# Optimization experiments

Hardware: AMD Instinct MI355X
Metric: run time of the kernel (lower is better)

Reference implementation:

```python
import jax, jax.numpy as jnp
import numpy as np

BIT_SHIFT = 8
H, W = 480, 640
N = 100000
C_IN, C_HID, C_OUT = 96, 576, 96


def setup_inputs() -> dict:
    key = jax.random.key(0)
    ks = jax.random.split(key, 12)
    # --- sparse 2D coordinates (unique active sites on an H x W grid) ---
    rng = np.random.default_rng(0)
    lin = rng.choice(H * W, size=N, replace=False)
    ys, xs = lin // W, lin % W
    grid = -np.ones((H, W), dtype=np.int32)
    grid[ys, xs] = np.arange(N, dtype=np.int32)
    # neighbor index for each of the 9 kernel offsets; -1 where no active neighbor
    nbr = np.empty((9, N), dtype=np.int32)
    k = 0
    for dy in (-1, 0, 1):
        for dx in (-1, 0, 1):
            yn, xn = ys + dy, xs + dx
            valid = (yn >= 0) & (yn < H) & (xn >= 0) & (xn < W)
            idx = grid[np.clip(yn, 0, H - 1), np.clip(xn, 0, W - 1)]
            nbr[k] = np.where(valid, idx, -1)
            k += 1
    # --- int8-valued float features / weights (quantized integer inference) ---
    feats = jnp.round(jnp.clip(30.0 * jax.random.normal(ks[0], (N, C_IN)), -127, 127))
    w1 = jnp.round(jnp.clip(40.0 * jax.random.normal(ks[1], (C_IN, C_HID)), -127, 127))
    b1 = jnp.round(1000.0 * jax.random.normal(ks[2], (C_HID,)))
    w2 = jnp.round(jnp.clip(40.0 * jax.random.normal(ks[3], (9, C_HID)), -127, 127))
    b2 = jnp.round(1000.0 * jax.random.normal(ks[4], (C_HID,)))
    w3 = jnp.round(jnp.clip(40.0 * jax.random.normal(ks[5], (C_HID, C_OUT)), -127, 127))
    b3 = jnp.round(1000.0 * jax.random.normal(ks[6], (C_OUT,)))
    # per-output-channel requantization scaling factors (>= ~1 so round() is nonzero)
    s1 = 1.0 + 3.0 * jax.random.uniform(ks[7], (C_HID,))
    s2 = 1.0 + 3.0 * jax.random.uniform(ks[8], (C_HID,))
    s3 = 1.0 + 3.0 * jax.random.uniform(ks[9], (C_OUT,))
    s_main = 1.0 + 2.0 * jax.random.uniform(ks[10], ())
    s_res = 1.0 + 2.0 * jax.random.uniform(ks[11], ())
    return {"feats": feats, "neighbor_idx": jnp.asarray(nbr), "w1": w1, "b1": b1,
            "w2": w2, "b2": b2, "w3": w3, "b3": b3,
            "s1": s1, "s2": s2, "s3": s3, "s_main": s_main, "s_res": s_res}


def _requant(acc, s):
    # fused integer rescale: multiplier m = round(s) * 2^bit_shift, then /2^(2*bit_shift)
    B = 2.0 ** BIT_SHIFT
    return acc * (jnp.round(s) * B) / (B * B)


def _clamp(x):
    lim = 2.0 ** (BIT_SHIFT - 1)
    return jnp.clip(x, -lim, lim)


def _relu6(x):
    return jnp.clip(x, 0.0, 6.0)


def reference(feats, neighbor_idx, w1, b1, w2, b2, w3, b3, s1, s2, s3, s_main, s_res):
    B = 2.0 ** BIT_SHIFT
    # 1x1 expand conv (dense GEMM over active sites)
    x = _relu6(_clamp(_requant(feats @ w1 + b1, s1)))  # [N, C_HID]
    # depthwise 3x3 sparse conv: gather 9 neighbor taps, mask missing sites
    mask = (neighbor_idx >= 0).astype(x.dtype)               # [9, N]
    gathered = x[jnp.clip(neighbor_idx, 0, None)] * mask[:, :, None]  # [9, N, C_HID]
    dw = jnp.einsum('knc,kc->nc', gathered, w2) + b2
    x = _relu6(_clamp(_requant(dw, s2)))
    # 1x1 project conv
    x = _clamp(_requant(x @ w3 + b3, s3))                    # [N, C_OUT]
    # scaled residual add
    out = jnp.round(s_main) * B * x + jnp.round(s_res) * B * feats
    return out
```

## Files before the change

### kernel.cpp

```cpp
#include <hip/hip_runtime.h>
#include <hip/hip_bf16.h>
#include <hip/hip_fp16.h>

#define NS   100000
#define CIN  96
#define CHID 576
#define COUT 96
#define SPB  48
#define LDH  (CHID + 8)
#define CPT  8
#define NG   (CHID / CPT)
#define NSLOT (576 / NG)
#define SPS  (SPB / NSLOT)

typedef float    floatx4 __attribute__((ext_vector_type(4)));
typedef int      intx4   __attribute__((ext_vector_type(4)));
typedef short    short8  __attribute__((ext_vector_type(8)));
typedef _Float16 half8   __attribute__((ext_vector_type(8)));
typedef _Float16 half4   __attribute__((ext_vector_type(4)));

__global__ void prep_kernel(const float* __restrict__ w1, const float* __restrict__ w3,
                            const float* __restrict__ w2,
                            unsigned short* __restrict__ w1T, _Float16* __restrict__ w3T,
                            _Float16* __restrict__ w2h, _Float16* __restrict__ x1h) {
  int i = blockIdx.x * blockDim.x + threadIdx.x;
  if (i >= CHID * CIN) return;
  if (i < CHID) x1h[(size_t)NS * CHID + i] = (_Float16)0.0f;
  if (i < 9 * CHID) w2h[i] = (_Float16)w2[i];
  {
    int h = i / CIN, k = i % CIN;
    w1T[i] = (unsigned short)(__float_as_uint(w1[k * CHID + h]) >> 16);
  }
  {
    int o = i / CHID, k = i % CHID;
    w3T[i] = (_Float16)w3[k * COUT + o];
  }
}

__global__ __launch_bounds__(64) void expand_kernel(
    const float* __restrict__ feats, const float* __restrict__ b1,
    const float* __restrict__ s1, const unsigned short* __restrict__ w1T,
    _Float16* __restrict__ x1h) {
  const int lane = threadIdx.x;
  const int m = lane & 15, quad = lane >> 4;
  const int s0 = blockIdx.x * 64;

  short8 bfrag[4][3];
#pragma unroll
  for (int u = 0; u < 4; ++u) {
    const int site = min(s0 + u * 16 + m, NS - 1);
    const float* frow = feats + (size_t)site * CIN + quad * 8;
#pragma unroll
    for (int kc = 0; kc < 3; ++kc) {
      const float4 lo = *reinterpret_cast<const float4*>(frow + kc * 32);
      const float4 hi = *reinterpret_cast<const float4*>(frow + kc * 32 + 4);
      const float v[8] = {lo.x, lo.y, lo.z, lo.w, hi.x, hi.y, hi.z, hi.w};
#pragma unroll
      for (int j = 0; j < 8; ++j)
        bfrag[u][kc][j] = (short)(__float_as_uint(v[j]) >> 16);
    }
  }

  const int hq = quad * 4;
#pragma unroll 2
  for (int ht = 0; ht < CHID / 16; ++ht) {
    const unsigned short* wrow = w1T + (ht * 16 + m) * CIN + quad * 8;
    short8 a[3];
#pragma unroll
    for (int kc = 0; kc < 3; ++kc)
      a[kc] = *reinterpret_cast<const short8*>(wrow + kc * 32);

    floatx4 acc[4] = {{0.f, 0.f, 0.f, 0.f}, {0.f, 0.f, 0.f, 0.f},
                      {0.f, 0.f, 0.f, 0.f}, {0.f, 0.f, 0.f, 0.f}};
#pragma unroll
    for (int kc = 0; kc < 3; ++kc)
#pragma unroll
      for (int u = 0; u < 4; ++u)
        acc[u] = __builtin_amdgcn_mfma_f32_16x16x32_bf16(a[kc], bfrag[u][kc], acc[u], 0, 0, 0);

    const floatx4 bv = *reinterpret_cast<const floatx4*>(b1 + ht * 16 + hq);
    const floatx4 sv = *reinterpret_cast<const floatx4*>(s1 + ht * 16 + hq);
    floatx4 sc;
#pragma unroll
    for (int j = 0; j < 4; ++j) sc[j] = rintf(sv[j]) * (1.0f / 256.0f);

#pragma unroll
    for (int u = 0; u < 4; ++u) {
      const int site = s0 + u * 16 + m;
      if (site < NS) {
        half4 r;
#pragma unroll
        for (int j = 0; j < 4; ++j) {
          float v = (acc[u][j] + bv[j]) * sc[j];
          r[j] = (_Float16)fminf(fmaxf(v, 0.0f), 6.0f);
        }
        *reinterpret_cast<half4*>(x1h + (size_t)site * CHID + ht * 16 + hq) = r;
      }
    }
  }
}

__global__ __launch_bounds__(576) void dwproj_kernel(
    const int* __restrict__ nbr, const _Float16* __restrict__ w2h,
    const float* __restrict__ b2, const float* __restrict__ s2,
    const _Float16* __restrict__ x1h, const _Float16* __restrict__ w3T,
    const float* __restrict__ feats, const float* __restrict__ b3,
    const float* __restrict__ s3, const float* __restrict__ s_main,
    const float* __restrict__ s_res, float* __restrict__ out) {
  __shared__ _Float16 x2t[SPB * LDH];
  __shared__ int offt[SPB * 12];
  const int t = threadIdx.x;
  const int s0 = blockIdx.x * SPB;

  if (t < SPB * 9) {
    const int k = t / SPB, n = t - k * SPB;
    const int site = min(s0 + n, NS - 1);
    const int idx = nbr[k * NS + site];
    offt[n * 12 + k] = (idx < 0 ? NS : idx) * CHID;
  }
  __syncthreads();

  {
    const int g = t % NG;
    const int slot = t / NG;
    const int c0 = g * CPT;
    half8 wv[9];
#pragma unroll
    for (int k = 0; k < 9; ++k)
      wv[k] = *reinterpret_cast<const half8*>(w2h + k * CHID + c0);
    float bvv[8], scv[8];
    {
      const floatx4 b0 = *reinterpret_cast<const floatx4*>(b2 + c0);
      const floatx4 b1v = *reinterpret_cast<const floatx4*>(b2 + c0 + 4);
      const floatx4 sa = *reinterpret_cast<const floatx4*>(s2 + c0);
      const floatx4 sb = *reinterpret_cast<const floatx4*>(s2 + c0 + 4);
#pragma unroll
      for (int j = 0; j < 4; ++j) {
        bvv[j] = b0[j];     bvv[j + 4] = b1v[j];
        scv[j] = rintf(sa[j]) * (1.0f / 256.0f);
        scv[j + 4] = rintf(sb[j]) * (1.0f / 256.0f);
      }
    }
#pragma unroll 2
    for (int i = 0; i < SPS; ++i) {
      const int n = slot * SPS + i;
      const intx4 oa = *reinterpret_cast<const intx4*>(offt + n * 12);
      const intx4 ob = *reinterpret_cast<const intx4*>(offt + n * 12 + 4);
      const int o8 = offt[n * 12 + 8];
      half8 v0 = *reinterpret_cast<const half8*>(x1h + (size_t)oa.x + c0);
      half8 v1 = *reinterpret_cast<const half8*>(x1h + (size_t)oa.y + c0);
      half8 v2 = *reinterpret_cast<const half8*>(x1h + (size_t)oa.z + c0);
      half8 v3 = *reinterpret_cast<const half8*>(x1h + (size_t)oa.w + c0);
      half8 v4 = *reinterpret_cast<const half8*>(x1h + (size_t)ob.x + c0);
      half8 v5 = *reinterpret_cast<const half8*>(x1h + (size_t)ob.y + c0);
      half8 v6 = *reinterpret_cast<const half8*>(x1h + (size_t)ob.z + c0);
      half8 v7 = *reinterpret_cast<const half8*>(x1h + (size_t)ob.w + c0);
      half8 v8 = *reinterpret_cast<const half8*>(x1h + (size_t)o8 + c0);
      float acc[8];
#pragma unroll
      for (int j = 0; j < 8; ++j) acc[j] = bvv[j];
#pragma unroll
      for (int j = 0; j < 8; ++j) {
        acc[j] += (float)v0[j] * (float)wv[0][j];
        acc[j] += (float)v1[j] * (float)wv[1][j];
        acc[j] += (float)v2[j] * (float)wv[2][j];
        acc[j] += (float)v3[j] * (float)wv[3][j];
        acc[j] += (float)v4[j] * (float)wv[4][j];
        acc[j] += (float)v5[j] * (float)wv[5][j];
        acc[j] += (float)v6[j] * (float)wv[6][j];
        acc[j] += (float)v7[j] * (float)wv[7][j];
        acc[j] += (float)v8[j] * (float)wv[8][j];
      }
      half8 r;
#pragma unroll
      for (int j = 0; j < 8; ++j) {
        float v = acc[j] * scv[j];
        r[j] = (_Float16)fminf(fmaxf(v, 0.0f), 6.0f);
      }
      *reinterpret_cast<half8*>(x2t + n * LDH + c0) = r;
    }
  }
  __syncthreads();

  const int wave = t >> 6, lane = t & 63;
  const int m = lane & 15, quad = lane >> 4;
  const float rsm = rintf(s_main[0]) * 256.0f;
  const float rsr = rintf(s_res[0]) * 256.0f;

  for (int tile = wave; tile < (SPB / 16) * (COUT / 16); tile += 9) {
    const int tm = tile / (COUT / 16);
    const int ot = tile % (COUT / 16);
    floatx4 acc = {0.f, 0.f, 0.f, 0.f};
    const _Float16* arow = w3T + (ot * 16 + m) * CHID + quad * 8;
    const _Float16* blds = x2t + (tm * 16 + m) * LDH + quad * 8;
#pragma unroll
    for (int kc = 0; kc < 18; ++kc) {
      const half8 a = *reinterpret_cast<const half8*>(arow + kc * 32);
      const half8 b = *reinterpret_cast<const half8*>(blds + kc * 32);
      acc = __builtin_amdgcn_mfma_f32_16x16x32_f16(a, b, acc, 0, 0, 0);
    }
    const int site = s0 + tm * 16 + m;
    if (site < NS) {
      const int o0 = ot * 16 + quad * 4;
      const floatx4 b3v = *reinterpret_cast<const floatx4*>(b3 + o0);
      const floatx4 s3v = *reinterpret_cast<const floatx4*>(s3 + o0);
      const floatx4 fv =
          *reinterpret_cast<const floatx4*>(feats + (size_t)site * COUT + o0);
      floatx4 r;
#pragma unroll
      for (int j = 0; j < 4; ++j) {
        float v = (acc[j] + b3v[j]) * (rintf(s3v[j]) * (1.0f / 256.0f));
        v = fminf(fmaxf(v, -128.0f), 128.0f);
        r[j] = rsm * v + rsr * fv[j];
      }
      *reinterpret_cast<floatx4*>(out + (size_t)site * COUT + o0) = r;
    }
  }
}

extern "C" void kernel_launch(void* const* d_in, const int* in_sizes, int n_in,
                              void* d_out, int out_size, void* d_ws, size_t ws_size,
                              hipStream_t stream) {
  const float* feats  = (const float*)d_in[0];
  const int*   nbr    = (const int*)d_in[1];
  const float* w1     = (const float*)d_in[2];
  const float* b1     = (const float*)d_in[3];
  const float* w2     = (const float*)d_in[4];
  const float* b2     = (const float*)d_in[5];
  const float* w3     = (const float*)d_in[6];
  const float* b3     = (const float*)d_in[7];
  const float* s1     = (const float*)d_in[8];
  const float* s2     = (const float*)d_in[9];
  const float* s3     = (const float*)d_in[10];
  const float* s_main = (const float*)d_in[11];
  const float* s_res  = (const float*)d_in[12];
  float* out = (float*)d_out;

  char* ws = (char*)d_ws;
  _Float16*       x1h = (_Float16*)ws;
  unsigned short* w1T = (unsigned short*)(ws + 115201152);
  _Float16*       w3T = (_Float16*)(ws + 115311744);
  _Float16*       w2h = (_Float16*)(ws + 115422336);

  prep_kernel<<<(CHID * CIN + 255) / 256, 256, 0, stream>>>(w1, w3, w2, w1T, w3T, w2h, x1h);
  expand_kernel<<<(NS + 63) / 64, 64, 0, stream>>>(feats, b1, s1, w1T, x1h);
  const int nblk = (NS + SPB - 1) / SPB;
  dwproj_kernel<<<nblk, 576, 0, stream>>>(nbr, w2h, b2, s2, x1h, w3T,
                                          feats, b3, s3, s_main, s_res, out);
}
```

Before: 332.8 us.

## Stage expand output in LDS for coalesced stores, split hidden tiles across waves

The expand kernel now runs four waves per block, each computing a quarter of the hidden channels, and stages the FP16 results in shared memory before writing full rows to global memory with wide coalesced stores. This replaces the scattered 8-byte stores of the single-wave version. The depthwise/projection kernel drops from 48 to 32 sites per block and removes the bounds checks, relying on NS being divisible by 32. The cost is extra LDS traffic and a barrier in expand, and the hard-coded divisibility assumption.

```diff
diff --git a/kernel.cpp b/kernel.cpp
--- a/kernel.cpp
+++ b/kernel.cpp
@@ -6,8 +6,9 @@
 #define CIN  96
 #define CHID 576
 #define COUT 96
-#define SPB  48
+#define SPB  32
 #define LDH  (CHID + 8)
+#define LDXR (CHID + 8)
 #define CPT  8
 #define NG   (CHID / CPT)
 #define NSLOT (576 / NG)
@@ -37,11 +38,13 @@
   }
 }
 
-__global__ __launch_bounds__(64) void expand_kernel(
+__global__ __launch_bounds__(256) void expand_kernel(
     const float* __restrict__ feats, const float* __restrict__ b1,
     const float* __restrict__ s1, const unsigned short* __restrict__ w1T,
     _Float16* __restrict__ x1h) {
-  const int lane = threadIdx.x;
+  __shared__ _Float16 x1t[64 * LDXR];
+  const int t = threadIdx.x;
+  const int wave = t >> 6, lane = t & 63;
   const int m = lane & 15, quad = lane >> 4;
   const int s0 = blockIdx.x * 64;
 
@@ -62,8 +65,9 @@
   }
 
   const int hq = quad * 4;
-#pragma unroll 2
-  for (int ht = 0; ht < CHID / 16; ++ht) {
+  const int ht0 = wave * 9;
+#pragma unroll 3
+  for (int ht = ht0; ht < ht0 + 9; ++ht) {
     const unsigned short* wrow = w1T + (ht * 16 + m) * CIN + quad * 8;
     short8 a[3];
 #pragma unroll
@@ -86,17 +90,25 @@
 
 #pragma unroll
     for (int u = 0; u < 4; ++u) {
-      const int site = s0 + u * 16 + m;
-      if (site < NS) {
-        half4 r;
-#pragma unroll
-        for (int j = 0; j < 4; ++j) {
-          float v = (acc[u][j] + bv[j]) * sc[j];
-          r[j] = (_Float16)fminf(fmaxf(v, 0.0f), 6.0f);
-        }
-        *reinterpret_cast<half4*>(x1h + (size_t)site * CHID + ht * 16 + hq) = r;
-      }
-    }
+      half4 r;
+#pragma unroll
+      for (int j = 0; j < 4; ++j) {
+        float v = (acc[u][j] + bv[j]) * sc[j];
+        r[j] = (_Float16)fminf(fmaxf(v, 0.0f), 6.0f);
+      }
+      *reinterpret_cast<half4*>(x1t + (u * 16 + m) * LDXR + ht * 16 + hq) = r;
+    }
+  }
+  __syncthreads();
+
+  const int r = t >> 2, sub = t & 3;
+  if (s0 + r < NS) {
+    _Float16* dst = x1h + (size_t)(s0 + r) * CHID + sub * 144;
+    const _Float16* src = x1t + r * LDXR + sub * 144;
+#pragma unroll
+    for (int i = 0; i < 18; ++i)
+      *reinterpret_cast<half8*>(dst + i * 8) =
+          *reinterpret_cast<const half8*>(src + i * 8);
   }
 }
 
@@ -113,9 +125,8 @@
   const int s0 = blockIdx.x * SPB;
 
   if (t < SPB * 9) {
-    const int k = t / SPB, n = t - k * SPB;
-    const int site = min(s0 + n, NS - 1);
-    const int idx = nbr[k * NS + site];
+    const int k = t >> 5, n = t & 31;
+    const int idx = nbr[k * NS + s0 + n];
     offt[n * 12 + k] = (idx < 0 ? NS : idx) * CHID;
   }
   __syncthreads();
@@ -200,21 +211,19 @@
       acc = __builtin_amdgcn_mfma_f32_16x16x32_f16(a, b, acc, 0, 0, 0);
     }
     const int site = s0 + tm * 16 + m;
-    if (site < NS) {
-      const int o0 = ot * 16 + quad * 4;
-      const floatx4 b3v = *reinterpret_cast<const floatx4*>(b3 + o0);
-      const floatx4 s3v = *reinterpret_cast<const floatx4*>(s3 + o0);
-      const floatx4 fv =
-          *reinterpret_cast<const floatx4*>(feats + (size_t)site * COUT + o0);
-      floatx4 r;
-#pragma unroll
-      for (int j = 0; j < 4; ++j) {
-        float v = (acc[j] + b3v[j]) * (rintf(s3v[j]) * (1.0f / 256.0f));
-        v = fminf(fmaxf(v, -128.0f), 128.0f);
-        r[j] = rsm * v + rsr * fv[j];
-      }
-      *reinterpret_cast<floatx4*>(out + (size_t)site * COUT + o0) = r;
-    }
+    const int o0 = ot * 16 + quad * 4;
+    const floatx4 b3v = *reinterpret_cast<const floatx4*>(b3 + o0);
+    const floatx4 s3v = *reinterpret_cast<const floatx4*>(s3 + o0);
+    const floatx4 fv =
+        *reinterpret_cast<const floatx4*>(feats + (size_t)site * COUT + o0);
+    floatx4 r;
+#pragma unroll
+    for (int j = 0; j < 4; ++j) {
+      float v = (acc[j] + b3v[j]) * (rintf(s3v[j]) * (1.0f / 256.0f));
+      v = fminf(fmaxf(v, -128.0f), 128.0f);
+      r[j] = rsm * v + rsr * fv[j];
+    }
+    *reinterpret_cast<floatx4*>(out + (size_t)site * COUT + o0) = r;
   }
 }
 
@@ -243,8 +252,7 @@
   _Float16*       w2h = (_Float16*)(ws + 115422336);
 
   prep_kernel<<<(CHID * CIN + 255) / 256, 256, 0, stream>>>(w1, w3, w2, w1T, w3T, w2h, x1h);
-  expand_kernel<<<(NS + 63) / 64, 64, 0, stream>>>(feats, b1, s1, w1T, x1h);
-  const int nblk = (NS + SPB - 1) / SPB;
-  dwproj_kernel<<<nblk, 576, 0, stream>>>(nbr, w2h, b2, s2, x1h, w3T,
-                                          feats, b3, s3, s_main, s_res, out);
-}
+  expand_kernel<<<(NS + 63) / 64, 256, 0, stream>>>(feats, b1, s1, w1T, x1h);
+  dwproj_kernel<<<NS / SPB, 576, 0, stream>>>(nbr, w2h, b2, s2, x1h, w3T,
+                                              feats, b3, s3, s_main, s_res, out);
+}
```

Measured after the change: 361.0 us. 1.08x slower.
